# Kernel optimization log

Hardware: AMD Instinct MI355X
Metric: run time of the kernel (lower is better)

The kernel has to match this reference:

```python
import jax, jax.numpy as jnp
import numpy as np

B, S, D = 16, 4096, 64


def setup_inputs() -> dict:
    key = jax.random.key(0)
    kq, kk, kv = jax.random.split(key, 3)
    q = jax.random.normal(kq, (B, S, D), dtype=jnp.float32)
    k = jax.random.normal(kk, (B, S, D), dtype=jnp.float32)
    v = jax.random.normal(kv, (B, S, D), dtype=jnp.float32)
    inv_scale_factor = jnp.float32(1.0 / np.sqrt(D))  # source DIVIDES by this
    p = 0  # dropout prob (deterministic baseline -> identity)
    return {"q": q, "k": k, "v": v, "inv_scale_factor": inv_scale_factor, "p": p}


def reference(q, k, v, inv_scale_factor, p):
    # qk = q @ k^T ; scaled = qk / inv_scale_factor (faithful to source)
    scores = jnp.einsum("bsd,btd->bst", q, k) / inv_scale_factor  # [B,S,S]
    attn = jax.nn.softmax(scores, axis=-1)
    # dropout with p=0 is identity (eval-mode baseline)
    out = jnp.einsum("bst,btd->bsd", attn, v)  # [B,S,D]
    return out
```

## Files before the change

### kernel.cpp

```cpp
#include <hip/hip_runtime.h>
#include <hip/hip_bf16.h>

typedef float f32x4 __attribute__((ext_vector_type(4)));
typedef float f32x16 __attribute__((ext_vector_type(16)));
typedef _Float16 half8 __attribute__((ext_vector_type(8)));
typedef __bf16 bf16x8 __attribute__((ext_vector_type(8)));
typedef __bf16 bf16x4 __attribute__((ext_vector_type(4)));
typedef unsigned short ushort_t;

constexpr int Bb = 16, Ss = 4096, Dd = 64;
constexpr int KBLK = 32, QBLK = 128;
constexpr int NT = Ss / KBLK;
constexpr float kLOG2E = 1.44269504088896340736f;
constexpr float DEFER_THR = 10.0f;

constexpr int KP_BLOCKS = (Bb * Ss * Dd / 8) / 256;
constexpr int VT_BLOCKS = (Bb * Dd * (Ss / 32)) / 256;

#define GLOAD_LDS16(gp, lp)                                                              \
    __builtin_amdgcn_global_load_lds(                                                    \
        (const __attribute__((address_space(1))) void*)(gp),                             \
        (__attribute__((address_space(3))) void*)(lp), 16, 0, 0)

__global__ __launch_bounds__(256)
void prep_f16s(const float* __restrict__ K, const float* __restrict__ V,
               _Float16* __restrict__ Khi, _Float16* __restrict__ Klo,
               _Float16* __restrict__ Vt)
{
    const int bid = blockIdx.x;
    if (bid < KP_BLOCKS) {
        const size_t idx = ((size_t)bid * 256 + threadIdx.x) * 8;
        const float4 a = *reinterpret_cast<const float4*>(K + idx);
        const float4 c = *reinterpret_cast<const float4*>(K + idx + 4);
        float xs[8] = {a.x, a.y, a.z, a.w, c.x, c.y, c.z, c.w};
        half8 h8, l8;
#pragma unroll
        for (int i = 0; i < 8; ++i) {
            const _Float16 h = (_Float16)xs[i];
            h8[i] = h;
            l8[i] = (_Float16)(xs[i] - (float)h);
        }
        *reinterpret_cast<half8*>(Khi + idx) = h8;
        *reinterpret_cast<half8*>(Klo + idx) = l8;
    } else {
        const int t = (bid - KP_BLOCKS) * 256 + threadIdx.x;
        const int d = t & 63;
        const int s32 = (t >> 6) & (Ss / 32 - 1);
        const int b = t >> 13;
        const float* vp = V + ((size_t)b * Ss + (size_t)s32 * 32) * Dd + d;
        __align__(16) _Float16 ob[32];
#pragma unroll
        for (int j = 0; j < 32; ++j) ob[j] = (_Float16)vp[(size_t)j * Dd];
        _Float16* op = Vt + ((size_t)b * Dd + d) * Ss + (size_t)s32 * 32;
#pragma unroll
        for (int j8 = 0; j8 < 4; ++j8)
            *reinterpret_cast<half8*>(op + j8 * 8) = *reinterpret_cast<half8*>(ob + j8 * 8);
    }
}

union H8 { half8 h; unsigned int u[4]; };

__global__ __launch_bounds__(512, 4)
void attn_fwd_v14(const float* __restrict__ Q, const float* __restrict__ inv_scale,
                  const _Float16* __restrict__ Khi, const _Float16* __restrict__ Klo,
                  const _Float16* __restrict__ Vt, float* __restrict__ Out)
{
    __shared__ __align__(16) unsigned char smem[48 * 1024];

    const int tid = threadIdx.x;
    const int lane = tid & 63;
    const int w = tid >> 6;
    const int p = w & 1;
    const int qg = w >> 1;
    const int l31 = lane & 31;
    const int hi = lane >> 5;

    const int bid = (blockIdx.x & 7) * 64 + (blockIdx.x >> 3);
    const int b = bid >> 5;
    const int q0 = (bid & 31) * QBLK;

    const _Float16* KhB = Khi + (size_t)b * Ss * Dd;
    const _Float16* KlB = Klo + (size_t)b * Ss * Dd;
    const _Float16* VB = Vt + (size_t)b * Dd * Ss;

    const int c = tid & 255;
    const int kk = c >> 3;
    const int ksrc = kk * Dd + (((c & 7) ^ (kk & 7)) << 3);
    const int dd_ = c >> 2;
    const size_t vsrc = (size_t)dd_ * Ss + (((c & 3) ^ ((dd_ >> 1) & 3)) << 3);

#define STAGE(t)                                                                            \
    do {                                                                                    \
        const int _sl = (t) & 3;                                                            \
        if (tid < 256) {                                                                    \
            GLOAD_LDS16(KhB + (size_t)(t) * (KBLK * Dd) + ksrc,                             \
                        smem + _sl * 4096 + c * 16);                                        \
            GLOAD_LDS16(KlB + (size_t)(t) * (KBLK * Dd) + ksrc,                             \
                        smem + 16384 + _sl * 4096 + c * 16);                                \
        } else {                                                                            \
            GLOAD_LDS16(VB + (size_t)(t) * KBLK + vsrc,                                     \
                        smem + 32768 + _sl * 4096 + c * 16);                                \
        }                                                                                   \
    } while (0)

    STAGE(0);
    STAGE(1);

    int koff[4], voff[4];
#pragma unroll
    for (int ks = 0; ks < 4; ++ks)
        koff[ks] = l31 * 128 + ((((ks << 1) + hi) ^ (l31 & 7)) << 4);
#pragma unroll
    for (int i = 0; i < 4; ++i) {
        const int d = (i >> 1) * 32 + l31;
        voff[i] = d * 64 + (((((i & 1) << 1) + hi) ^ ((d >> 1) & 3)) << 4);
    }

    H8 qhi[4], qlo[4];
    {
        const float s2 = (1.0f / inv_scale[0]) * kLOG2E;
        const float* qrow = Q + ((size_t)b * Ss + q0 + qg * 32 + l31) * Dd;
#pragma unroll
        for (int ks = 0; ks < 4; ++ks) {
            const int d0 = ks * 16 + hi * 8;
            const float4 a = *reinterpret_cast<const float4*>(qrow + d0);
            const float4 cc = *reinterpret_cast<const float4*>(qrow + d0 + 4);
            float xs[8] = {a.x, a.y, a.z, a.w, cc.x, cc.y, cc.z, cc.w};
#pragma unroll
            for (int i = 0; i < 8; ++i) {
                const float x = xs[i] * s2;
                const _Float16 h = (_Float16)x;
                qhi[ks].h[i] = h;
                qlo[ks].h[i] = (_Float16)(x - (float)h);
            }
        }
    }

    f32x16 O0, O1;
#pragma unroll
    for (int r = 0; r < 16; ++r) { O0[r] = 0.f; O1[r] = 0.f; }
    float m_run = -INFINITY, l_run = 0.f;

    __syncthreads();

    for (int it = 0; it < NT / 2; ++it) {
        const int t = 2 * it + p;
        const unsigned char* khbase = smem + (t & 3) * 4096;
        const unsigned char* klbase = smem + 16384 + (t & 3) * 4096;
        const unsigned char* vbase = smem + 32768 + (t & 3) * 4096;

        if (it < NT / 2 - 1) { STAGE(2 * it + 2); STAGE(2 * it + 3); }

        f32x16 S;
#pragma unroll
        for (int r = 0; r < 16; ++r) S[r] = 0.f;
#pragma unroll
        for (int ks = 0; ks < 4; ++ks) {
            const half8 kh = *reinterpret_cast<const half8*>(khbase + koff[ks]);
            const half8 kl = *reinterpret_cast<const half8*>(klbase + koff[ks]);
            S = __builtin_amdgcn_mfma_f32_32x32x16_f16(kh, qhi[ks].h, S, 0, 0, 0);
            S = __builtin_amdgcn_mfma_f32_32x32x16_f16(kl, qhi[ks].h, S, 0, 0, 0);
            S = __builtin_amdgcn_mfma_f32_32x32x16_f16(kh, qlo[ks].h, S, 0, 0, 0);
        }

        float tmax = S[0];
#pragma unroll
        for (int r = 1; r < 16; ++r) tmax = fmaxf(tmax, S[r]);
        tmax = fmaxf(tmax, __shfl_xor(tmax, 32));

        float fac = 1.0f;
        if (__any(tmax > m_run + DEFER_THR)) {
            const float m_new = fmaxf(m_run, tmax);
            fac = __builtin_amdgcn_exp2f(m_run - m_new);
            m_run = m_new;
#pragma unroll
            for (int r = 0; r < 16; ++r) { O0[r] *= fac; O1[r] *= fac; }
        }

        float tsum = 0.f;
#pragma unroll
        for (int r = 0; r < 16; ++r) {
            S[r] = __builtin_amdgcn_exp2f(S[r] - m_run);
            tsum += S[r];
        }
        tsum += __shfl_xor(tsum, 32);
        l_run = l_run * fac + tsum;

        unsigned int wd[8];
#pragma unroll
        for (int j = 0; j < 8; ++j) {
            const auto h2 = __builtin_amdgcn_cvt_pkrtz(S[2 * j], S[2 * j + 1]);
            wd[j] = __builtin_bit_cast(unsigned int, h2);
        }
        auto xhalf = [&](unsigned int& a, unsigned int& cx) {
            const unsigned int y = hi ? a : cx;
            const unsigned int sy = __shfl_xor(y, 32);
            const unsigned int na = hi ? sy : a;
            const unsigned int nc = hi ? cx : sy;
            a = na; cx = nc;
        };
        xhalf(wd[0], wd[2]);
        xhalf(wd[1], wd[3]);
        xhalf(wd[4], wd[6]);
        xhalf(wd[5], wd[7]);

        H8 pf0, pf1;
        pf0.u[0] = wd[0]; pf0.u[1] = wd[1]; pf0.u[2] = wd[2]; pf0.u[3] = wd[3];
        pf1.u[0] = wd[4]; pf1.u[1] = wd[5]; pf1.u[2] = wd[6]; pf1.u[3] = wd[7];

        O0 = __builtin_amdgcn_mfma_f32_32x32x16_f16(
            *reinterpret_cast<const half8*>(vbase + voff[0]), pf0.h, O0, 0, 0, 0);
        O0 = __builtin_amdgcn_mfma_f32_32x32x16_f16(
            *reinterpret_cast<const half8*>(vbase + voff[1]), pf1.h, O0, 0, 0, 0);
        O1 = __builtin_amdgcn_mfma_f32_32x32x16_f16(
            *reinterpret_cast<const half8*>(vbase + voff[2]), pf0.h, O1, 0, 0, 0);
        O1 = __builtin_amdgcn_mfma_f32_32x32x16_f16(
            *reinterpret_cast<const half8*>(vbase + voff[3]), pf1.h, O1, 0, 0, 0);

        __syncthreads();
    }

    float* mO = (float*)smem;
    float* ml = (float*)(smem + 32768);

    if (p == 1) {
#pragma unroll
        for (int dblk = 0; dblk < 2; ++dblk)
#pragma unroll
            for (int rr = 0; rr < 4; ++rr) {
                f32x4 v;
                if (dblk == 0) {
                    v[0] = O0[rr * 4 + 0]; v[1] = O0[rr * 4 + 1];
                    v[2] = O0[rr * 4 + 2]; v[3] = O0[rr * 4 + 3];
                } else {
                    v[0] = O1[rr * 4 + 0]; v[1] = O1[rr * 4 + 1];
                    v[2] = O1[rr * 4 + 2]; v[3] = O1[rr * 4 + 3];
                }
                *reinterpret_cast<f32x4*>(mO + (((qg * 2 + dblk) * 4 + rr) << 8) + lane * 4) = v;
            }
        if (hi == 0) {
            ml[qg * 64 + l31] = m_run;
            ml[qg * 64 + 32 + l31] = l_run;
        }
    }
    __syncthreads();
    if (p == 0) {
        const float m1 = ml[qg * 64 + l31];
        const float l1 = ml[qg * 64 + 32 + l31];
        const float mm = fmaxf(m_run, m1);
        float f0 = __builtin_amdgcn_exp2f(m_run - mm);
        float f1 = __builtin_amdgcn_exp2f(m1 - mm);
        const float inv = 1.0f / (l_run * f0 + l1 * f1);
        f0 *= inv; f1 *= inv;
        float* orow = Out + ((size_t)b * Ss + q0 + qg * 32 + l31) * Dd;
#pragma unroll
        for (int dblk = 0; dblk < 2; ++dblk)
#pragma unroll
            for (int rr = 0; rr < 4; ++rr) {
                const f32x4 ov = *reinterpret_cast<const f32x4*>(
                    mO + (((qg * 2 + dblk) * 4 + rr) << 8) + lane * 4);
                f32x4 res;
#pragma unroll
                for (int j = 0; j < 4; ++j) {
                    const float mine = (dblk == 0) ? O0[rr * 4 + j] : O1[rr * 4 + j];
                    res[j] = mine * f0 + ov[j] * f1;
                }
                *reinterpret_cast<f32x4*>(orow + dblk * 32 + rr * 8 + hi * 4) = res;
            }
    }
#undef STAGE
}

__global__ __launch_bounds__(256)
void attn_fwd_fallback(const float* __restrict__ Q, const float* __restrict__ K,
                       const float* __restrict__ V, const float* __restrict__ inv_scale,
                       float* __restrict__ Out)
{
    __shared__ __align__(16) ushort_t sKhi[KBLK * Dd];
    __shared__ __align__(16) ushort_t sKlo[KBLK * Dd];
    __shared__ __align__(16) ushort_t sVt[Dd * KBLK];
    __shared__ __align__(16) ushort_t sP[4][16 * KBLK];

    const int tid = threadIdx.x;
    const int lane = tid & 63;
    const int w = tid >> 6;
    const int q15 = lane & 15;
    const int g = lane >> 4;
    const int b = blockIdx.x >> 6;
    const int q0 = (blockIdx.x & 63) * 64;
    const float scale = 1.0f / inv_scale[0];

    const float* qptr = Q + (((size_t)b * Ss) + q0 + w * 16 + q15) * Dd;
    bf16x8 qhi[2], qlo[2];
#pragma unroll
    for (int ds = 0; ds < 2; ++ds) {
        const float4 f0 = *reinterpret_cast<const float4*>(qptr + ds * 32 + g * 8);
        const float4 f1 = *reinterpret_cast<const float4*>(qptr + ds * 32 + g * 8 + 4);
        float xs[8] = {f0.x, f0.y, f0.z, f0.w, f1.x, f1.y, f1.z, f1.w};
#pragma unroll
        for (int i = 0; i < 8; ++i) {
            __bf16 h = (__bf16)xs[i];
            qhi[ds][i] = h;
            qlo[ds][i] = (__bf16)(xs[i] - (float)h);
        }
    }
    const int krs = tid >> 3;
    const int kc8 = (tid & 7) * 8;
    const int kidx = krs * Dd + (kc8 ^ ((krs & 7) << 3));
    const float* kbase = K + ((size_t)b * Ss) * Dd;
    const int vd = tid & 63;
    const int vk8 = (tid >> 6) * 8;
    const int vidx = vd * KBLK + (vk8 ^ ((vd & 3) << 3));
    const float* vbase = V + ((size_t)b * Ss) * Dd;

    f32x4 Oacc[4];
#pragma unroll
    for (int dt = 0; dt < 4; ++dt)
#pragma unroll
        for (int r = 0; r < 4; ++r) Oacc[dt][r] = 0.f;
    float m_run = -INFINITY, l_run = 0.f;

    for (int k0 = 0; k0 < Ss; k0 += KBLK) {
        {
            const float* p0 = kbase + (size_t)(k0 + krs) * Dd + kc8;
            const float4 a = *reinterpret_cast<const float4*>(p0);
            const float4 c = *reinterpret_cast<const float4*>(p0 + 4);
            float xs[8] = {a.x, a.y, a.z, a.w, c.x, c.y, c.z, c.w};
            bf16x8 h8, l8;
#pragma unroll
            for (int i = 0; i < 8; ++i) {
                __bf16 h = (__bf16)xs[i];
                h8[i] = h;
                l8[i] = (__bf16)(xs[i] - (float)h);
            }
            *reinterpret_cast<bf16x8*>(&sKhi[kidx]) = h8;
            *reinterpret_cast<bf16x8*>(&sKlo[kidx]) = l8;
        }
        {
            bf16x8 v8;
#pragma unroll
            for (int j = 0; j < 8; ++j) v8[j] = (__bf16)vbase[(size_t)(k0 + vk8 + j) * Dd + vd];
            *reinterpret_cast<bf16x8*>(&sVt[vidx]) = v8;
        }
        __syncthreads();

        float z[2][4];
#pragma unroll
        for (int t = 0; t < 2; ++t) {
            const int krow = t * 16 + q15;
            f32x4 acc;
            acc[0] = acc[1] = acc[2] = acc[3] = 0.f;
#pragma unroll
            for (int ds = 0; ds < 2; ++ds) {
                const int ci = (ds * 32 + g * 8) ^ ((krow & 7) << 3);
                const bf16x8 kh = *reinterpret_cast<const bf16x8*>(&sKhi[krow * Dd + ci]);
                const bf16x8 kl = *reinterpret_cast<const bf16x8*>(&sKlo[krow * Dd + ci]);
                acc = __builtin_amdgcn_mfma_f32_16x16x32_bf16(kh, qhi[ds], acc, 0, 0, 0);
                acc = __builtin_amdgcn_mfma_f32_16x16x32_bf16(kl, qhi[ds], acc, 0, 0, 0);
                acc = __builtin_amdgcn_mfma_f32_16x16x32_bf16(kh, qlo[ds], acc, 0, 0, 0);
            }
#pragma unroll
            for (int r = 0; r < 4; ++r) z[t][r] = acc[r] * scale;
        }

        float tmax = z[0][0];
#pragma unroll
        for (int t = 0; t < 2; ++t)
#pragma unroll
            for (int r = 0; r < 4; ++r) tmax = fmaxf(tmax, z[t][r]);
        tmax = fmaxf(tmax, __shfl_xor(tmax, 16));
        tmax = fmaxf(tmax, __shfl_xor(tmax, 32));
        const float m_new = fmaxf(m_run, tmax);

        float pz[2][4];
        float tsum = 0.f;
#pragma unroll
        for (int t = 0; t < 2; ++t)
#pragma unroll
            for (int r = 0; r < 4; ++r) {
                const float e = __builtin_amdgcn_exp2f((z[t][r] - m_new) * kLOG2E);
                pz[t][r] = e;
                tsum += e;
            }
        tsum += __shfl_xor(tsum, 16);
        tsum += __shfl_xor(tsum, 32);
        const float fac = __builtin_amdgcn_exp2f((m_run - m_new) * kLOG2E);
        l_run = l_run * fac + tsum;
        m_run = m_new;

#pragma unroll
        for (int t = 0; t < 2; ++t) {
            bf16x4 pb;
#pragma unroll
            for (int r = 0; r < 4; ++r) pb[r] = (__bf16)pz[t][r];
            const int pidx = q15 * KBLK + ((t * 16 + g * 4) ^ ((q15 & 3) << 3));
            *reinterpret_cast<bf16x4*>(&sP[w][pidx]) = pb;
        }
        {
            const float fr0 = __shfl(fac, g * 4 + 0);
            const float fr1 = __shfl(fac, g * 4 + 1);
            const float fr2 = __shfl(fac, g * 4 + 2);
            const float fr3 = __shfl(fac, g * 4 + 3);
#pragma unroll
            for (int dt = 0; dt < 4; ++dt) {
                Oacc[dt][0] *= fr0; Oacc[dt][1] *= fr1;
                Oacc[dt][2] *= fr2; Oacc[dt][3] *= fr3;
            }
        }
        const int paidx = q15 * KBLK + ((g * 8) ^ ((q15 & 3) << 3));
        const bf16x8 pa = *reinterpret_cast<const bf16x8*>(&sP[w][paidx]);
#pragma unroll
        for (int dt = 0; dt < 4; ++dt) {
            const int dd = dt * 16 + q15;
            const bf16x8 vf =
                *reinterpret_cast<const bf16x8*>(&sVt[dd * KBLK + ((g * 8) ^ ((dd & 3) << 3))]);
            Oacc[dt] = __builtin_amdgcn_mfma_f32_16x16x32_bf16(pa, vf, Oacc[dt], 0, 0, 0);
        }
        __syncthreads();
    }

    const float invl = 1.0f / l_run;
    float il[4];
#pragma unroll
    for (int r = 0; r < 4; ++r) il[r] = __shfl(invl, g * 4 + r);
    float* obase = Out + (((size_t)b * Ss) + q0 + w * 16) * Dd;
#pragma unroll
    for (int dt = 0; dt < 4; ++dt)
#pragma unroll
        for (int r = 0; r < 4; ++r)
            obase[(size_t)(g * 4 + r) * Dd + dt * 16 + q15] = Oacc[dt][r] * il[r];
}

extern "C" void kernel_launch(void* const* d_in, const int* in_sizes, int n_in,
                              void* d_out, int out_size, void* d_ws, size_t ws_size,
                              hipStream_t stream)
{
    const float* q = (const float*)d_in[0];
    const float* k = (const float*)d_in[1];
    const float* v = (const float*)d_in[2];
    const float* inv_scale = (const float*)d_in[3];
    float* out = (float*)d_out;
    (void)in_sizes; (void)n_in; (void)out_size;

    const size_t NKV = (size_t)Bb * Ss * Dd;
    const size_t need = NKV * 3 * sizeof(_Float16);

    if (ws_size >= need) {
        _Float16* Khi = (_Float16*)d_ws;
        _Float16* Klo = Khi + NKV;
        _Float16* Vt = Klo + NKV;
        hipLaunchKernelGGL(prep_f16s, dim3(KP_BLOCKS + VT_BLOCKS), dim3(256), 0, stream,
                           k, v, Khi, Klo, Vt);
        hipLaunchKernelGGL(attn_fwd_v14, dim3(Bb * (Ss / QBLK)), dim3(512), 0, stream,
                           q, inv_scale, Khi, Klo, Vt, out);
    } else {
        hipLaunchKernelGGL(attn_fwd_fallback, dim3(Bb * 64), dim3(256), 0, stream,
                           q, k, v, inv_scale, out);
    }
}
```

Measured before the change: 169.3 us.

## Unroll KV loop by two with fixed LDS slots and pointer-increment staging

Manually unrolls the key-tile loop so each iteration processes two pairs of tiles using compile-time LDS slot offsets. Global-to-LDS staging now uses incrementing pointers instead of recomputed tile addresses. The first QK MFMA seeds from a zero accumulator and the max reduction becomes a tree. Launch bounds drop from 4 to 3 waves per SIMD, giving the compiler more registers at the cost of occupancy.

New measurement: 177.7 us. 1.05x slower.

```diff
diff --git a/kernel.cpp b/kernel.cpp
--- a/kernel.cpp
+++ b/kernel.cpp
@@ -11,6 +11,7 @@
 constexpr int Bb = 16, Ss = 4096, Dd = 64;
 constexpr int KBLK = 32, QBLK = 128;
 constexpr int NT = Ss / KBLK;
+constexpr int KD = KBLK * Dd;
 constexpr float kLOG2E = 1.44269504088896340736f;
 constexpr float DEFER_THR = 10.0f;
 
@@ -60,8 +61,8 @@
 
 union H8 { half8 h; unsigned int u[4]; };
 
-__global__ __launch_bounds__(512, 4)
-void attn_fwd_v14(const float* __restrict__ Q, const float* __restrict__ inv_scale,
+__global__ __launch_bounds__(512, 3)
+void attn_fwd_v15(const float* __restrict__ Q, const float* __restrict__ inv_scale,
                   const _Float16* __restrict__ Khi, const _Float16* __restrict__ Klo,
                   const _Float16* __restrict__ Vt, float* __restrict__ Out)
 {
@@ -89,22 +90,19 @@
     const int dd_ = c >> 2;
     const size_t vsrc = (size_t)dd_ * Ss + (((c & 3) ^ ((dd_ >> 1) & 3)) << 3);
 
-#define STAGE(t)                                                                            \
-    do {                                                                                    \
-        const int _sl = (t) & 3;                                                            \
-        if (tid < 256) {                                                                    \
-            GLOAD_LDS16(KhB + (size_t)(t) * (KBLK * Dd) + ksrc,                             \
-                        smem + _sl * 4096 + c * 16);                                        \
-            GLOAD_LDS16(KlB + (size_t)(t) * (KBLK * Dd) + ksrc,                             \
-                        smem + 16384 + _sl * 4096 + c * 16);                                \
-        } else {                                                                            \
-            GLOAD_LDS16(VB + (size_t)(t) * KBLK + vsrc,                                     \
-                        smem + 32768 + _sl * 4096 + c * 16);                                \
-        }                                                                                   \
-    } while (0)
-
-    STAGE(0);
-    STAGE(1);
+    if (tid < 256) {
+        GLOAD_LDS16(KhB + ksrc, smem + c * 16);
+        GLOAD_LDS16(KhB + ksrc + KD, smem + 4096 + c * 16);
+        GLOAD_LDS16(KlB + ksrc, smem + 16384 + c * 16);
+        GLOAD_LDS16(KlB + ksrc + KD, smem + 16384 + 4096 + c * 16);
+    } else {
+        GLOAD_LDS16(VB + vsrc, smem + 32768 + c * 16);
+        GLOAD_LDS16(VB + vsrc + KBLK, smem + 32768 + 4096 + c * 16);
+    }
+
+    const _Float16* khp = KhB + ksrc + 2 * KD;
+    const _Float16* klp = KlB + ksrc + 2 * KD;
+    const _Float16* vpp = VB + vsrc + 2 * KBLK;
 
     int koff[4], voff[4];
 #pragma unroll
@@ -136,89 +134,116 @@
         }
     }
 
-    f32x16 O0, O1;
-#pragma unroll
-    for (int r = 0; r < 16; ++r) { O0[r] = 0.f; O1[r] = 0.f; }
+    f32x16 O0, O1, ZACC;
+#pragma unroll
+    for (int r = 0; r < 16; ++r) { O0[r] = 0.f; O1[r] = 0.f; ZACC[r] = 0.f; }
     float m_run = -INFINITY, l_run = 0.f;
 
     __syncthreads();
 
-    for (int it = 0; it < NT / 2; ++it) {
-        const int t = 2 * it + p;
-        const unsigned char* khbase = smem + (t & 3) * 4096;
-        const unsigned char* klbase = smem + 16384 + (t & 3) * 4096;
-        const unsigned char* vbase = smem + 32768 + (t & 3) * 4096;
-
-        if (it < NT / 2 - 1) { STAGE(2 * it + 2); STAGE(2 * it + 3); }
-
-        f32x16 S;
-#pragma unroll
-        for (int r = 0; r < 16; ++r) S[r] = 0.f;
-#pragma unroll
-        for (int ks = 0; ks < 4; ++ks) {
-            const half8 kh = *reinterpret_cast<const half8*>(khbase + koff[ks]);
-            const half8 kl = *reinterpret_cast<const half8*>(klbase + koff[ks]);
-            S = __builtin_amdgcn_mfma_f32_32x32x16_f16(kh, qhi[ks].h, S, 0, 0, 0);
-            S = __builtin_amdgcn_mfma_f32_32x32x16_f16(kl, qhi[ks].h, S, 0, 0, 0);
-            S = __builtin_amdgcn_mfma_f32_32x32x16_f16(kh, qlo[ks].h, S, 0, 0, 0);
-        }
-
-        float tmax = S[0];
-#pragma unroll
-        for (int r = 1; r < 16; ++r) tmax = fmaxf(tmax, S[r]);
-        tmax = fmaxf(tmax, __shfl_xor(tmax, 32));
-
-        float fac = 1.0f;
-        if (__any(tmax > m_run + DEFER_THR)) {
-            const float m_new = fmaxf(m_run, tmax);
-            fac = __builtin_amdgcn_exp2f(m_run - m_new);
-            m_run = m_new;
-#pragma unroll
-            for (int r = 0; r < 16; ++r) { O0[r] *= fac; O1[r] *= fac; }
-        }
-
-        float tsum = 0.f;
-#pragma unroll
-        for (int r = 0; r < 16; ++r) {
-            S[r] = __builtin_amdgcn_exp2f(S[r] - m_run);
-            tsum += S[r];
-        }
-        tsum += __shfl_xor(tsum, 32);
-        l_run = l_run * fac + tsum;
-
-        unsigned int wd[8];
-#pragma unroll
-        for (int j = 0; j < 8; ++j) {
-            const auto h2 = __builtin_amdgcn_cvt_pkrtz(S[2 * j], S[2 * j + 1]);
-            wd[j] = __builtin_bit_cast(unsigned int, h2);
-        }
-        auto xhalf = [&](unsigned int& a, unsigned int& cx) {
-            const unsigned int y = hi ? a : cx;
-            const unsigned int sy = __shfl_xor(y, 32);
-            const unsigned int na = hi ? sy : a;
-            const unsigned int nc = hi ? cx : sy;
-            a = na; cx = nc;
-        };
-        xhalf(wd[0], wd[2]);
-        xhalf(wd[1], wd[3]);
-        xhalf(wd[4], wd[6]);
-        xhalf(wd[5], wd[7]);
-
-        H8 pf0, pf1;
-        pf0.u[0] = wd[0]; pf0.u[1] = wd[1]; pf0.u[2] = wd[2]; pf0.u[3] = wd[3];
-        pf1.u[0] = wd[4]; pf1.u[1] = wd[5]; pf1.u[2] = wd[6]; pf1.u[3] = wd[7];
-
-        O0 = __builtin_amdgcn_mfma_f32_32x32x16_f16(
-            *reinterpret_cast<const half8*>(vbase + voff[0]), pf0.h, O0, 0, 0, 0);
-        O0 = __builtin_amdgcn_mfma_f32_32x32x16_f16(
-            *reinterpret_cast<const half8*>(vbase + voff[1]), pf1.h, O0, 0, 0, 0);
-        O1 = __builtin_amdgcn_mfma_f32_32x32x16_f16(
-            *reinterpret_cast<const half8*>(vbase + voff[2]), pf0.h, O1, 0, 0, 0);
-        O1 = __builtin_amdgcn_mfma_f32_32x32x16_f16(
-            *reinterpret_cast<const half8*>(vbase + voff[3]), pf1.h, O1, 0, 0, 0);
-
+#define PROCESS(SL)                                                                        \
+    do {                                                                                   \
+        const unsigned char* khbase = smem + (SL) * 4096;                                  \
+        const unsigned char* klbase = smem + 16384 + (SL) * 4096;                          \
+        const unsigned char* vbase = smem + 32768 + (SL) * 4096;                           \
+        const half8 kh0 = *reinterpret_cast<const half8*>(khbase + koff[0]);               \
+        const half8 kl0 = *reinterpret_cast<const half8*>(klbase + koff[0]);               \
+        f32x16 S = __builtin_amdgcn_mfma_f32_32x32x16_f16(kh0, qhi[0].h, ZACC, 0, 0, 0);   \
+        S = __builtin_amdgcn_mfma_f32_32x32x16_f16(kl0, qhi[0].h, S, 0, 0, 0);             \
+        S = __builtin_amdgcn_mfma_f32_32x32x16_f16(kh0, qlo[0].h, S, 0, 0, 0);             \
+        _Pragma("unroll") for (int ks = 1; ks < 4; ++ks) {                                 \
+            const half8 kh = *reinterpret_cast<const half8*>(khbase + koff[ks]);           \
+            const half8 kl = *reinterpret_cast<const half8*>(klbase + koff[ks]);           \
+            S = __builtin_amdgcn_mfma_f32_32x32x16_f16(kh, qhi[ks].h, S, 0, 0, 0);         \
+            S = __builtin_amdgcn_mfma_f32_32x32x16_f16(kl, qhi[ks].h, S, 0, 0, 0);         \
+            S = __builtin_amdgcn_mfma_f32_32x32x16_f16(kh, qlo[ks].h, S, 0, 0, 0);         \
+        }                                                                                  \
+                                                        \
+        const float a0 = fmaxf(fmaxf(S[0], S[1]), S[2]);                                   \
+        const float a1 = fmaxf(fmaxf(S[3], S[4]), S[5]);                                   \
+        const float a2 = fmaxf(fmaxf(S[6], S[7]), S[8]);                                   \
+        const float a3 = fmaxf(fmaxf(S[9], S[10]), S[11]);                                 \
+        const float a4 = fmaxf(fmaxf(S[12], S[13]), S[14]);                                \
+        const float b0 = fmaxf(fmaxf(a0, a1), a2);                                         \
+        const float b1 = fmaxf(fmaxf(a3, a4), S[15]);                                      \
+        float tmax = fmaxf(b0, b1);                                                        \
+        tmax = fmaxf(tmax, __shfl_xor(tmax, 32));                                          \
+        float fac = 1.0f;                                                                  \
+        if (__any(tmax > m_run + DEFER_THR)) {                                             \
+            const float m_new = fmaxf(m_run, tmax);                                        \
+            fac = __builtin_amdgcn_exp2f(m_run - m_new);                                   \
+            m_run = m_new;                                                                 \
+            _Pragma("unroll") for (int r = 0; r < 16; ++r) { O0[r] *= fac; O1[r] *= fac; } \
+        }                                                                                  \
+        float tsum = 0.f;                                                                  \
+        _Pragma("unroll") for (int r = 0; r < 16; ++r) {                                   \
+            S[r] = __builtin_amdgcn_exp2f(S[r] - m_run);                                   \
+            tsum += S[r];                                                                  \
+        }                                                                                  \
+        tsum += __shfl_xor(tsum, 32);                                                      \
+        l_run = l_run * fac + tsum;                                                        \
+        unsigned int wd[8];                                                                \
+        _Pragma("unroll") for (int j = 0; j < 8; ++j) {                                    \
+            const auto h2 = __builtin_amdgcn_cvt_pkrtz(S[2 * j], S[2 * j + 1]);            \
+            wd[j] = __builtin_bit_cast(unsigned int, h2);                                  \
+        }                                                                                  \
+        xhalf(wd[0], wd[2]);                                                               \
+        xhalf(wd[1], wd[3]);                                                               \
+        xhalf(wd[4], wd[6]);                                                               \
+        xhalf(wd[5], wd[7]);                                                               \
+        H8 pf0, pf1;                                                                       \
+        pf0.u[0] = wd[0]; pf0.u[1] = wd[1]; pf0.u[2] = wd[2]; pf0.u[3] = wd[3];            \
+        pf1.u[0] = wd[4]; pf1.u[1] = wd[5]; pf1.u[2] = wd[6]; pf1.u[3] = wd[7];            \
+        O0 = __builtin_amdgcn_mfma_f32_32x32x16_f16(                                       \
+            *reinterpret_cast<const half8*>(vbase + voff[0]), pf0.h, O0, 0, 0, 0);         \
+        O0 = __builtin_amdgcn_mfma_f32_32x32x16_f16(                                       \
+            *reinterpret_cast<const half8*>(vbase + voff[1]), pf1.h, O0, 0, 0, 0);         \
+        O1 = __builtin_amdgcn_mfma_f32_32x32x16_f16(                                       \
+            *reinterpret_cast<const half8*>(vbase + voff[2]), pf0.h, O1, 0, 0, 0);         \
+        O1 = __builtin_amdgcn_mfma_f32_32x32x16_f16(                                       \
+            *reinterpret_cast<const half8*>(vbase + voff[3]), pf1.h, O1, 0, 0, 0);         \
+    } while (0)
+
+    auto xhalf = [&](unsigned int& a, unsigned int& cx) {
+        const unsigned int y = hi ? a : cx;
+        const unsigned int sy = __shfl_xor(y, 32);
+        const unsigned int na = hi ? sy : a;
+        const unsigned int nc = hi ? cx : sy;
+        a = na; cx = nc;
+    };
+
+    for (int ih = 0; ih < 32; ++ih) {
+        if (tid < 256) {
+            GLOAD_LDS16(khp, smem + 2 * 4096 + c * 16);
+            GLOAD_LDS16(khp + KD, smem + 3 * 4096 + c * 16);
+            GLOAD_LDS16(klp, smem + 16384 + 2 * 4096 + c * 16);
+            GLOAD_LDS16(klp + KD, smem + 16384 + 3 * 4096 + c * 16);
+        } else {
+            GLOAD_LDS16(vpp, smem + 32768 + 2 * 4096 + c * 16);
+            GLOAD_LDS16(vpp + KBLK, smem + 32768 + 3 * 4096 + c * 16);
+        }
+        PROCESS(p);
         __syncthreads();
-    }
+
+        if (ih < 31) {
+            if (tid < 256) {
+                GLOAD_LDS16(khp + 2 * KD, smem + c * 16);
+                GLOAD_LDS16(khp + 3 * KD, smem + 4096 + c * 16);
+                GLOAD_LDS16(klp + 2 * KD, smem + 16384 + c * 16);
+                GLOAD_LDS16(klp + 3 * KD, smem + 16384 + 4096 + c * 16);
+            } else {
+                GLOAD_LDS16(vpp + 2 * KBLK, smem + 32768 + c * 16);
+                GLOAD_LDS16(vpp + 3 * KBLK, smem + 32768 + 4096 + c * 16);
+            }
+        }
+        PROCESS(2 + p);
+        __syncthreads();
+
+        khp += 4 * KD;
+        klp += 4 * KD;
+        vpp += 4 * KBLK;
+    }
+#undef PROCESS
 
     float* mO = (float*)smem;
     float* ml = (float*)(smem + 32768);
@@ -268,7 +293,6 @@
                 *reinterpret_cast<f32x4*>(orow + dblk * 32 + rr * 8 + hi * 4) = res;
             }
     }
-#undef STAGE
 }
 
 __global__ __launch_bounds__(256)
@@ -451,7 +475,7 @@
         _Float16* Vt = Klo + NKV;
         hipLaunchKernelGGL(prep_f16s, dim3(KP_BLOCKS + VT_BLOCKS), dim3(256), 0, stream,
                            k, v, Khi, Klo, Vt);
-        hipLaunchKernelGGL(attn_fwd_v14, dim3(Bb * (Ss / QBLK)), dim3(512), 0, stream,
+        hipLaunchKernelGGL(attn_fwd_v15, dim3(Bb * (Ss / QBLK)), dim3(512), 0, stream,
                            q, inv_scale, Khi, Klo, Vt, out);
     } else {
         hipLaunchKernelGGL(attn_fwd_fallback, dim3(Bb * 64), dim3(256), 0, stream,
```
